# Optimization experiments

Hardware: AMD Instinct MI355X
Metric: run time of the kernel (lower is better)

Reference implementation:

```python
import jax, jax.numpy as jnp
import numpy as np

CHANNELS = 1024
T_LEN = 16384
WINDOW = 16
W_MIN, W_MAX = -1.0, 3.0
BETA = 0.95       # snn.Leaky(beta=0.95)
THRESHOLD = 1.0   # snn.Leaky(threshold=1)


def setup_inputs() -> dict:
    key = jax.random.key(0)
    inp = jax.random.normal(key, (CHANNELS, T_LEN), dtype=jnp.float32)
    return {"inp": inp}


def reference(inp):
    C, T = inp.shape
    pad = WINDOW // 2
    inp_padded = jnp.pad(inp, ((0, 0), (pad, pad)))  # [C, T + WINDOW]
    n_steps = T - WINDOW

    def step(carry, t):
        w, mem = carry
        # B: sliding window [C, WINDOW] starting at column t of padded input
        B = jax.lax.dynamic_slice(inp_padded, (0, t), (C, WINDOW))
        # mean(B @ B.T, axis=1) == B @ mean(B, axis=0)  -- avoids [C, C] intermediate
        B_ram = B @ jnp.mean(B, axis=0)
        w = jnp.clip(0.5 * w + 0.5 * B_ram, W_MIN, W_MAX)
        x = B[:, 0]  # == inp_padded[:, t]
        # snntorch Leaky, reset_mechanism='subtract':
        # reset from incoming mem, then mem = beta*mem + input - reset*thr, spk = mem > thr
        reset = (mem > THRESHOLD).astype(inp.dtype)
        mem = BETA * mem + w * x - reset * THRESHOLD
        spk = (mem > THRESHOLD).astype(inp.dtype)
        return (w, mem), spk

    w0 = jnp.ones((C,), dtype=inp.dtype)
    mem0 = jnp.zeros((C,), dtype=inp.dtype)
    _, spks = jax.lax.scan(step, (w0, mem0), jnp.arange(n_steps))  # spks: [n_steps, C]
    # out = deepcopy(inp); out[:, t] = spk for t < T - WINDOW
    out = inp.at[:, :n_steps].set(spks.T)
    return out
```

## Files before the change

kernel.cpp:

```cpp
#include <hip/hip_runtime.h>

#define C_CH   1024
#define T_DIM  16384
#define NSTEPS (T_DIM - 16)
#define PAD    8
#define TP     (T_DIM + 16)
#define CHUNK  128
#define NCHUNK 128
#define WARM   256
#define XPADW  21
#define SPADW  21

#define WS_CM_OFFSET (8u * T_DIM * sizeof(double))

__global__ void colsum_partial(const float* __restrict__ inp, double* __restrict__ part) {
    int col4 = (blockIdx.x * 256 + threadIdx.x) * 4;
    int rc   = blockIdx.y;
    const float* p = inp + (size_t)rc * 128 * T_DIM + col4;
    double ax = 0.0, ay = 0.0, az = 0.0, aw = 0.0;
    #pragma unroll 4
    for (int r = 0; r < 128; ++r) {
        float4 v = *(const float4*)(p + (size_t)r * T_DIM);
        ax += (double)v.x; ay += (double)v.y; az += (double)v.z; aw += (double)v.w;
    }
    double* q = part + (size_t)rc * T_DIM + col4;
    q[0] = ax; q[1] = ay; q[2] = az; q[3] = aw;
}

__global__ void colmean_tail(const double* __restrict__ part, const float* __restrict__ inp,
                             float* __restrict__ cm, float* __restrict__ out) {
    int i = blockIdx.x * 256 + threadIdx.x;
    if (i < TP) {
        float v = 0.0f;
        if (i >= PAD && i < T_DIM + PAD) {
            int col = i - PAD;
            double t = 0.0;
            #pragma unroll
            for (int r = 0; r < 8; ++r) t += part[(size_t)r * T_DIM + col];
            v = (float)(t * (1.0 / 1024.0));
        }
        cm[i] = v;
    }
    if (i < C_CH * 16) {
        int c = i >> 4, j = i & 15;
        size_t idx = (size_t)c * T_DIM + NSTEPS + j;
        out[idx] = inp[idx];
    }
}

__global__ __launch_bounds__(64) void scan_kernel(const float* __restrict__ inp,
                                                  const float* __restrict__ cm,
                                                  float* __restrict__ out) {
    __shared__ float xt[64][XPADW];
    __shared__ float st[64][SPADW];

    const int k    = blockIdx.x;
    const int lane = threadIdx.x;
    const int c0   = blockIdx.y * 64;
    const int t0   = k * CHUNK;
    const int tend = min(t0 + CHUNK, NSTEPS);
    const int tw   = (t0 - WARM > 0) ? (t0 - WARM) : 0;

    const float* row = inp + (size_t)(c0 + lane) * T_DIM;

    const int sr  = lane >> 2;
    const int sc4 = (lane & 3) << 2;
    const float* srow0 = inp + (size_t)(c0 + sr)      * T_DIM + sc4 + 8;
    const float* srow1 = inp + (size_t)(c0 + sr + 16) * T_DIM + sc4 + 8;
    const float* srow2 = inp + (size_t)(c0 + sr + 32) * T_DIM + sc4 + 8;
    const float* srow3 = inp + (size_t)(c0 + sr + 48) * T_DIM + sc4 + 8;
    float* orow0 = out + (size_t)(c0 + sr)      * T_DIM + sc4;
    float* orow1 = out + (size_t)(c0 + sr + 16) * T_DIM + sc4;
    float* orow2 = out + (size_t)(c0 + sr + 32) * T_DIM + sc4;
    float* orow3 = out + (size_t)(c0 + sr + 48) * T_DIM + sc4;

    float xs[16];
    float win = 0.0f;
    #pragma unroll
    for (int j = 0; j < 16; ++j) {
        int s = tw + j;
        float x = (s >= PAD) ? row[s - PAD] : 0.0f;
        xs[j] = x;
        win = fmaf(x, cm[s], win);
    }

    float w = 1.0f, mem = 0.0f;

    float4 r0 = *(const float4*)(srow0 + tw);
    float4 r1 = *(const float4*)(srow1 + tw);
    float4 r2 = *(const float4*)(srow2 + tw);
    float4 r3 = *(const float4*)(srow3 + tw);

    for (int t = tw; t < tend; t += 16) {
        xt[sr][sc4+0]    = r0.x; xt[sr][sc4+1]    = r0.y; xt[sr][sc4+2]    = r0.z; xt[sr][sc4+3]    = r0.w;
        xt[sr+16][sc4+0] = r1.x; xt[sr+16][sc4+1] = r1.y; xt[sr+16][sc4+2] = r1.z; xt[sr+16][sc4+3] = r1.w;
        xt[sr+32][sc4+0] = r2.x; xt[sr+32][sc4+1] = r2.y; xt[sr+32][sc4+2] = r2.z; xt[sr+32][sc4+3] = r2.w;
        xt[sr+48][sc4+0] = r3.x; xt[sr+48][sc4+1] = r3.y; xt[sr+48][sc4+2] = r3.z; xt[sr+48][sc4+3] = r3.w;
        __syncthreads();

        int ts = (t + 16 < tend) ? (t + 16) : t;
        r0 = *(const float4*)(srow0 + ts);
        r1 = *(const float4*)(srow1 + ts);
        r2 = *(const float4*)(srow2 + ts);
        r3 = *(const float4*)(srow3 + ts);

        #pragma unroll
        for (int j = 0; j < 16; ++j) {
            w = fminf(fmaxf(fmaf(0.5f, w, 0.5f * win), -1.0f), 3.0f);
            float x   = xs[j];
            float rst = (mem > 1.0f) ? 1.0f : 0.0f;
            mem = fmaf(0.95f, mem, fmaf(w, x, -rst));
            st[lane][j] = (mem > 1.0f) ? 1.0f : 0.0f;
            float xn = xt[lane][j];
            win = fmaf(xn, cm[t + 16 + j], fmaf(-x, cm[t + j], win));
            xs[j] = xn;
        }
        __syncthreads();

        if (t >= t0) {
            *(float4*)(orow0 + t) = make_float4(st[sr][sc4],    st[sr][sc4+1],    st[sr][sc4+2],    st[sr][sc4+3]);
            *(float4*)(orow1 + t) = make_float4(st[sr+16][sc4], st[sr+16][sc4+1], st[sr+16][sc4+2], st[sr+16][sc4+3]);
            *(float4*)(orow2 + t) = make_float4(st[sr+32][sc4], st[sr+32][sc4+1], st[sr+32][sc4+2], st[sr+32][sc4+3]);
            *(float4*)(orow3 + t) = make_float4(st[sr+48][sc4], st[sr+48][sc4+1], st[sr+48][sc4+2], st[sr+48][sc4+3]);
        }
        __syncthreads();
    }
}

extern "C" void kernel_launch(void* const* d_in, const int* in_sizes, int n_in,
                              void* d_out, int out_size, void* d_ws, size_t ws_size,
                              hipStream_t stream) {
    const float* inp = (const float*)d_in[0];
    float* out = (float*)d_out;
    double* part = (double*)d_ws;
    float* cm = (float*)((char*)d_ws + WS_CM_OFFSET);

    colsum_partial<<<dim3(T_DIM / 1024, 8), 256, 0, stream>>>(inp, part);
    colmean_tail<<<dim3(65), 256, 0, stream>>>(part, inp, cm, out);
    scan_kernel<<<dim3(NCHUNK, C_CH / 64), 64, 0, stream>>>(inp, cm, out);
}
```

Before: 172.2 us.

## Lengthen scan chunks, widen blocks to 128 channels, restructure column-sum reduction

The scan kernel now processes 512-step chunks with 128-channel blocks, so the fixed 256-step warm-up is amortized over more output steps. The initial window load is staged through shared memory with coalesced float4 reads instead of strided per-lane loads. The column-sum kernel switches to one column per thread with eight independent double accumulators over 4x more blocks, giving more parallelism and memory-level concurrency. The price is a much smaller grid for the scan (256 blocks of 2 waves), which may leave the GPU underoccupied for what is a latency-bound serial recurrence.

New measurement: 161.3 us. 1.07x faster.

```diff
diff --git a/kernel.cpp b/kernel.cpp
--- a/kernel.cpp
+++ b/kernel.cpp
@@ -5,26 +5,30 @@
 #define NSTEPS (T_DIM - 16)
 #define PAD    8
 #define TP     (T_DIM + 16)
-#define CHUNK  128
-#define NCHUNK 128
+#define CHUNK  512
+#define NCHUNK 32
 #define WARM   256
-#define XPADW  21
-#define SPADW  21
+#define LPITCH 17
 
 #define WS_CM_OFFSET (8u * T_DIM * sizeof(double))
 
 __global__ void colsum_partial(const float* __restrict__ inp, double* __restrict__ part) {
-    int col4 = (blockIdx.x * 256 + threadIdx.x) * 4;
-    int rc   = blockIdx.y;
-    const float* p = inp + (size_t)rc * 128 * T_DIM + col4;
-    double ax = 0.0, ay = 0.0, az = 0.0, aw = 0.0;
-    #pragma unroll 4
-    for (int r = 0; r < 128; ++r) {
-        float4 v = *(const float4*)(p + (size_t)r * T_DIM);
-        ax += (double)v.x; ay += (double)v.y; az += (double)v.z; aw += (double)v.w;
+    int col = blockIdx.x * 256 + threadIdx.x;
+    int rc  = blockIdx.y;
+    const float* p = inp + (size_t)rc * 128 * T_DIM + col;
+    double a0=0,a1=0,a2=0,a3=0,a4=0,a5=0,a6=0,a7=0;
+    #pragma unroll
+    for (int r = 0; r < 128; r += 8) {
+        a0 += (double)p[(size_t)(r+0) * T_DIM];
+        a1 += (double)p[(size_t)(r+1) * T_DIM];
+        a2 += (double)p[(size_t)(r+2) * T_DIM];
+        a3 += (double)p[(size_t)(r+3) * T_DIM];
+        a4 += (double)p[(size_t)(r+4) * T_DIM];
+        a5 += (double)p[(size_t)(r+5) * T_DIM];
+        a6 += (double)p[(size_t)(r+6) * T_DIM];
+        a7 += (double)p[(size_t)(r+7) * T_DIM];
     }
-    double* q = part + (size_t)rc * T_DIM + col4;
-    q[0] = ax; q[1] = ay; q[2] = az; q[3] = aw;
+    part[(size_t)rc * T_DIM + col] = ((a0+a1)+(a2+a3)) + ((a4+a5)+(a6+a7));
 }
 
 __global__ void colmean_tail(const double* __restrict__ part, const float* __restrict__ inp,
@@ -48,54 +52,66 @@
     }
 }
 
-__global__ __launch_bounds__(64) void scan_kernel(const float* __restrict__ inp,
-                                                  const float* __restrict__ cm,
-                                                  float* __restrict__ out) {
-    __shared__ float xt[64][XPADW];
-    __shared__ float st[64][SPADW];
+__global__ __launch_bounds__(128) void scan_kernel(const float* __restrict__ inp,
+                                                   const float* __restrict__ cm,
+                                                   float* __restrict__ out) {
+    __shared__ float xt[128][LPITCH];
+    __shared__ float st[128][LPITCH];
 
     const int k    = blockIdx.x;
     const int lane = threadIdx.x;
-    const int c0   = blockIdx.y * 64;
+    const int c0   = blockIdx.y * 128;
     const int t0   = k * CHUNK;
     const int tend = min(t0 + CHUNK, NSTEPS);
     const int tw   = (t0 - WARM > 0) ? (t0 - WARM) : 0;
 
-    const float* row = inp + (size_t)(c0 + lane) * T_DIM;
-
     const int sr  = lane >> 2;
     const int sc4 = (lane & 3) << 2;
     const float* srow0 = inp + (size_t)(c0 + sr)      * T_DIM + sc4 + 8;
-    const float* srow1 = inp + (size_t)(c0 + sr + 16) * T_DIM + sc4 + 8;
-    const float* srow2 = inp + (size_t)(c0 + sr + 32) * T_DIM + sc4 + 8;
-    const float* srow3 = inp + (size_t)(c0 + sr + 48) * T_DIM + sc4 + 8;
+    const float* srow1 = inp + (size_t)(c0 + sr + 32) * T_DIM + sc4 + 8;
+    const float* srow2 = inp + (size_t)(c0 + sr + 64) * T_DIM + sc4 + 8;
+    const float* srow3 = inp + (size_t)(c0 + sr + 96) * T_DIM + sc4 + 8;
     float* orow0 = out + (size_t)(c0 + sr)      * T_DIM + sc4;
-    float* orow1 = out + (size_t)(c0 + sr + 16) * T_DIM + sc4;
-    float* orow2 = out + (size_t)(c0 + sr + 32) * T_DIM + sc4;
-    float* orow3 = out + (size_t)(c0 + sr + 48) * T_DIM + sc4;
+    float* orow1 = out + (size_t)(c0 + sr + 32) * T_DIM + sc4;
+    float* orow2 = out + (size_t)(c0 + sr + 64) * T_DIM + sc4;
+    float* orow3 = out + (size_t)(c0 + sr + 96) * T_DIM + sc4;
+
+    float4 r0, r1, r2, r3;
+    if (tw == 0 && sc4 < 8) {
+        r0 = r1 = r2 = r3 = make_float4(0.f, 0.f, 0.f, 0.f);
+    } else {
+        r0 = *(const float4*)(srow0 + tw - 16);
+        r1 = *(const float4*)(srow1 + tw - 16);
+        r2 = *(const float4*)(srow2 + tw - 16);
+        r3 = *(const float4*)(srow3 + tw - 16);
+    }
+    xt[sr][sc4+0]    = r0.x; xt[sr][sc4+1]    = r0.y; xt[sr][sc4+2]    = r0.z; xt[sr][sc4+3]    = r0.w;
+    xt[sr+32][sc4+0] = r1.x; xt[sr+32][sc4+1] = r1.y; xt[sr+32][sc4+2] = r1.z; xt[sr+32][sc4+3] = r1.w;
+    xt[sr+64][sc4+0] = r2.x; xt[sr+64][sc4+1] = r2.y; xt[sr+64][sc4+2] = r2.z; xt[sr+64][sc4+3] = r2.w;
+    xt[sr+96][sc4+0] = r3.x; xt[sr+96][sc4+1] = r3.y; xt[sr+96][sc4+2] = r3.z; xt[sr+96][sc4+3] = r3.w;
+    __syncthreads();
 
     float xs[16];
     float win = 0.0f;
     #pragma unroll
     for (int j = 0; j < 16; ++j) {
-        int s = tw + j;
-        float x = (s >= PAD) ? row[s - PAD] : 0.0f;
+        float x = xt[lane][j];
         xs[j] = x;
-        win = fmaf(x, cm[s], win);
+        win = fmaf(x, cm[tw + j], win);
     }
+    float w = 1.0f, mem = 0.0f;
+    __syncthreads();
 
-    float w = 1.0f, mem = 0.0f;
-
-    float4 r0 = *(const float4*)(srow0 + tw);
-    float4 r1 = *(const float4*)(srow1 + tw);
-    float4 r2 = *(const float4*)(srow2 + tw);
-    float4 r3 = *(const float4*)(srow3 + tw);
+    r0 = *(const float4*)(srow0 + tw);
+    r1 = *(const float4*)(srow1 + tw);
+    r2 = *(const float4*)(srow2 + tw);
+    r3 = *(const float4*)(srow3 + tw);
 
     for (int t = tw; t < tend; t += 16) {
         xt[sr][sc4+0]    = r0.x; xt[sr][sc4+1]    = r0.y; xt[sr][sc4+2]    = r0.z; xt[sr][sc4+3]    = r0.w;
-        xt[sr+16][sc4+0] = r1.x; xt[sr+16][sc4+1] = r1.y; xt[sr+16][sc4+2] = r1.z; xt[sr+16][sc4+3] = r1.w;
-        xt[sr+32][sc4+0] = r2.x; xt[sr+32][sc4+1] = r2.y; xt[sr+32][sc4+2] = r2.z; xt[sr+32][sc4+3] = r2.w;
-        xt[sr+48][sc4+0] = r3.x; xt[sr+48][sc4+1] = r3.y; xt[sr+48][sc4+2] = r3.z; xt[sr+48][sc4+3] = r3.w;
+        xt[sr+32][sc4+0] = r1.x; xt[sr+32][sc4+1] = r1.y; xt[sr+32][sc4+2] = r1.z; xt[sr+32][sc4+3] = r1.w;
+        xt[sr+64][sc4+0] = r2.x; xt[sr+64][sc4+1] = r2.y; xt[sr+64][sc4+2] = r2.z; xt[sr+64][sc4+3] = r2.w;
+        xt[sr+96][sc4+0] = r3.x; xt[sr+96][sc4+1] = r3.y; xt[sr+96][sc4+2] = r3.z; xt[sr+96][sc4+3] = r3.w;
         __syncthreads();
 
         int ts = (t + 16 < tend) ? (t + 16) : t;
@@ -119,9 +135,9 @@
 
         if (t >= t0) {
             *(float4*)(orow0 + t) = make_float4(st[sr][sc4],    st[sr][sc4+1],    st[sr][sc4+2],    st[sr][sc4+3]);
-            *(float4*)(orow1 + t) = make_float4(st[sr+16][sc4], st[sr+16][sc4+1], st[sr+16][sc4+2], st[sr+16][sc4+3]);
-            *(float4*)(orow2 + t) = make_float4(st[sr+32][sc4], st[sr+32][sc4+1], st[sr+32][sc4+2], st[sr+32][sc4+3]);
-            *(float4*)(orow3 + t) = make_float4(st[sr+48][sc4], st[sr+48][sc4+1], st[sr+48][sc4+2], st[sr+48][sc4+3]);
+            *(float4*)(orow1 + t) = make_float4(st[sr+32][sc4], st[sr+32][sc4+1], st[sr+32][sc4+2], st[sr+32][sc4+3]);
+            *(float4*)(orow2 + t) = make_float4(st[sr+64][sc4], st[sr+64][sc4+1], st[sr+64][sc4+2], st[sr+64][sc4+3]);
+            *(float4*)(orow3 + t) = make_float4(st[sr+96][sc4], st[sr+96][sc4+1], st[sr+96][sc4+2], st[sr+96][sc4+3]);
         }
         __syncthreads();
     }
@@ -135,7 +151,7 @@
     double* part = (double*)d_ws;
     float* cm = (float*)((char*)d_ws + WS_CM_OFFSET);
 
-    colsum_partial<<<dim3(T_DIM / 1024, 8), 256, 0, stream>>>(inp, part);
+    colsum_partial<<<dim3(T_DIM / 256, 8), 256, 0, stream>>>(inp, part);
     colmean_tail<<<dim3(65), 256, 0, stream>>>(part, inp, cm, out);
-    scan_kernel<<<dim3(NCHUNK, C_CH / 64), 64, 0, stream>>>(inp, cm, out);
+    scan_kernel<<<dim3(NCHUNK, C_CH / 128), 128, 0, stream>>>(inp, cm, out);
 }
```
